# Kernel optimization log

Measured on AMD Instinct MI355X. Metric: run time of the kernel, lower is better.

## Reference

```python
import jax, jax.numpy as jnp
import numpy as np

POOL_LEN = 256
EPS = 1e-5
WEIGHT_BITS = 2


def adaptive_avg_pool1d(x, out_len):
    """Faithful torch AdaptiveAvgPool1d: window i = [floor(i*L/out), ceil((i+1)*L/out)).
    Implemented via cumsum + static gathers (jit-friendly, vectorized)."""
    L = x.shape[-1]
    i = np.arange(out_len)
    starts = (i * L) // out_len
    ends = -((-(i + 1) * L) // out_len)  # integer ceil
    csum = jnp.cumsum(x, axis=-1)
    csum = jnp.concatenate([jnp.zeros(x.shape[:-1] + (1,), x.dtype), csum], axis=-1)
    counts = jnp.asarray(ends - starts, x.dtype)
    return (csum[..., ends] - csum[..., starts]) / counts


def quantize_weight(w, bits=WEIGHT_BITS):
    """2-bit symmetric uniform quantization, per-output-channel scale, STE."""
    qp = 2 ** (bits - 1) - 1          # +1
    qn = -(2 ** (bits - 1))           # -2
    scale = jnp.maximum(jnp.max(jnp.abs(w), axis=1, keepdims=True) / qp, 1e-8)
    w_q = jnp.clip(jnp.round(w / scale), qn, qp) * scale
    return w + jax.lax.stop_gradient(w_q - w)  # straight-through estimator


def setup_inputs() -> dict:
    key = jax.random.key(0)
    k1, k2, k3, kw = jax.random.split(key, 4)
    B = 64
    return {
        "stage1": jax.random.normal(k1, (B, 256, 5000), jnp.float32),
        "stage2": jax.random.normal(k2, (B, 128, 2500), jnp.float32),
        "stage3": jax.random.normal(k3, (B, 64, 625), jnp.float32),
        "alpha": jnp.ones((3,), jnp.float32) / 3.0,
        "weight": jax.random.normal(kw, (128, 448), jnp.float32) * 0.05,
        "bias": jnp.zeros((128,), jnp.float32),
        "gamma": jnp.ones((128,), jnp.float32),
        "beta": jnp.zeros((128,), jnp.float32),
    }


def reference(stage1, stage2, stage3, alpha, weight, bias, gamma, beta):
    w = jax.nn.softmax(alpha)
    s1 = adaptive_avg_pool1d(stage1, POOL_LEN) * w[0]
    s2 = adaptive_avg_pool1d(stage2, POOL_LEN) * w[1]
    s3 = adaptive_avg_pool1d(stage3, POOL_LEN) * w[2]
    fused = jnp.concatenate([s1, s2, s3], axis=1)  # (B, 448, 256)
    wq = quantize_weight(weight)
    y = jnp.einsum('oc,bcl->bol', wq, fused) + bias[None, :, None]  # (B, 128, 256)
    # BatchNorm1d (training mode: batch stats over N and L)
    mean = jnp.mean(y, axis=(0, 2))
    var = jnp.var(y, axis=(0, 2))
    yn = (y - mean[None, :, None]) * jax.lax.rsqrt(var + EPS)[None, :, None]
    yn = yn * gamma[None, :, None] + beta[None, :, None]
    act = jax.nn.elu(yn)
    return jnp.mean(act, axis=-1)  # (B, 128)
```

## Files before the change

### kernel.cpp

```cpp
#include <hip/hip_runtime.h>
#include <hip/hip_bf16.h>

#define EPSV 1e-5f

typedef __attribute__((ext_vector_type(8))) short short8v;
typedef __attribute__((ext_vector_type(4))) short short4v;
typedef __attribute__((ext_vector_type(4))) float float4v;

__device__ inline unsigned short f2bf(float x) {
  __hip_bfloat16 h = __float2bfloat16(x);
  return *reinterpret_cast<unsigned short*>(&h);
}
__device__ inline float bf2f(unsigned short b) {
  unsigned u = ((unsigned)b) << 16;
  float f;
  __builtin_memcpy(&f, &u, 4);
  return f;
}

template <int L, int MAXW, int OPL>
__device__ __forceinline__ void windows_from_seg(
    const float* __restrict__ seg, int lbase, float wst,
    unsigned short* __restrict__ outp, int lane) {
  int sbase = (lbase * L) >> 8;
  unsigned short res[OPL];
  #pragma unroll
  for (int oo = 0; oo < OPL; ++oo) {
    int l = lbase + lane * OPL + oo;
    int start = ((l * L) >> 8) - sbase;
    int end = (((l + 1) * L + 255) >> 8) - sbase;
    int width = end - start;
    float s = 0.f;
    #pragma unroll
    for (int i = 0; i < MAXW; ++i) {
      float v = seg[start + i];
      s += (i < width) ? v : 0.f;
    }
    res[oo] = f2bf(s / (float)width * wst);
  }
  if (OPL == 2) {
    unsigned pk = ((unsigned)res[1] << 16) | res[0];
    *(unsigned*)(outp + lane * 2) = pk;
  } else {
    unsigned pk0 = ((unsigned)res[1] << 16) | res[0];
    unsigned pk1 = ((unsigned)res[3] << 16) | res[2];
    unsigned long long pk = ((unsigned long long)pk1 << 32) | pk0;
    *(unsigned long long*)(outp + lane * 4) = pk;
  }
}

template <int L, int SPAN, int MAXW, int OPL>
__device__ __forceinline__ void pool_span2_vec(
    const float* __restrict__ pA, const float* __restrict__ pB,
    int lbA, int lbB, float wst,
    unsigned short* __restrict__ outA, unsigned short* __restrict__ outB,
    float* __restrict__ seg, int lane) {
  constexpr int S4 = SPAN / 4;
  constexpr int NLD = (S4 + 63) / 64;
  float4v rA[NLD], rB[NLD];
  const float4v* gA = (const float4v*)pA;
  const float4v* gB = (const float4v*)pB;
  #pragma unroll
  for (int j = 0; j < NLD; ++j) {
    int idx = lane + 64 * j;
    if (NLD * 64 == S4 || idx < S4) rA[j] = __builtin_nontemporal_load(gA + idx);
  }
  #pragma unroll
  for (int j = 0; j < NLD; ++j) {
    int idx = lane + 64 * j;
    if (NLD * 64 == S4 || idx < S4) rB[j] = __builtin_nontemporal_load(gB + idx);
  }
  if (lane < MAXW + 3) seg[SPAN + lane] = 0.f;
  #pragma unroll
  for (int j = 0; j < NLD; ++j) {
    int idx = lane + 64 * j;
    if (NLD * 64 == S4 || idx < S4) *(float4v*)&seg[idx * 4] = rA[j];
  }
  windows_from_seg<L, MAXW, OPL>(seg, lbA, wst, outA, lane);
  #pragma unroll
  for (int j = 0; j < NLD; ++j) {
    int idx = lane + 64 * j;
    if (NLD * 64 == S4 || idx < S4) *(float4v*)&seg[idx * 4] = rB[j];
  }
  windows_from_seg<L, MAXW, OPL>(seg, lbB, wst, outB, lane);
}

template <int L, int SPAN, int MAXW, int OPL>
__device__ __forceinline__ void pool_span_scalar(
    const float* __restrict__ spanp, int lbase, float wst,
    unsigned short* __restrict__ outp, float* __restrict__ seg, int lane) {
  constexpr int NLD = (SPAN + 63) / 64;
  if (lane < MAXW + 3) seg[SPAN + lane] = 0.f;
  #pragma unroll
  for (int j = 0; j < NLD; ++j) {
    int idx = lane + 64 * j;
    if (idx < SPAN) seg[idx] = __builtin_nontemporal_load(spanp + idx);
  }
  windows_from_seg<L, MAXW, OPL>(seg, lbase, wst, outp, lane);
}

__global__ __launch_bounds__(256) void pool_quant_kernel(
    const float* __restrict__ s1, const float* __restrict__ s2,
    const float* __restrict__ s3, const float* __restrict__ alpha,
    const float* __restrict__ w, unsigned short* __restrict__ fusedb,
    unsigned short* __restrict__ qbf, float* __restrict__ scales) {
  __shared__ float pool_lds[4][2524];
  int bid = blockIdx.x;
  int t = threadIdx.x;
  int wv = t >> 6, lane = t & 63;

  if (bid >= 6144) {
    int o = bid - 6144;
    const float* wr = w + o * 448;
    float m = 0.f;
    for (int c = t; c < 448; c += 256) m = fmaxf(m, fabsf(wr[c]));
    float* sm = pool_lds[0];
    for (int off = 32; off; off >>= 1) m = fmaxf(m, __shfl_down(m, off, 64));
    if ((t & 63) == 0) sm[t >> 6] = m;
    __syncthreads();
    m = fmaxf(fmaxf(sm[0], sm[1]), fmaxf(sm[2], sm[3]));
    float scale = fmaxf(m, 1e-8f);
    for (int c = t; c < 448; c += 256) {
      float q = rintf(wr[c] / scale);
      q = fminf(fmaxf(q, -2.f), 1.f);
      qbf[o * 448 + c] = f2bf(q);
    }
    if (t == 0) scales[o] = scale;
    return;
  }

  float a0 = alpha[0], a1 = alpha[1], a2 = alpha[2];
  float mx = fmaxf(a0, fmaxf(a1, a2));
  float e0 = expf(a0 - mx), e1 = expf(a1 - mx), e2 = expf(a2 - mx);
  float esum = e0 + e1 + e2;
  float* seg = pool_lds[wv];

  if (bid < 4096) {
    int rr = bid * 4 + wv;
    int b = rr >> 8, c = rr & 255;
    const float* rowp = s1 + ((size_t)b * 256 + c) * 5000;
    unsigned short* outp = fusedb + ((size_t)b * 448 + c) * 256;
    pool_span2_vec<5000, 2500, 21, 2>(rowp, rowp + 2500, 0, 128, e0 / esum,
                                      outp, outp + 128, seg, lane);
  } else if (bid < 5120) {
    int wt = (bid - 4096) * 4 + wv;
    int rA = wt * 2, rB = rA + 1;
    int bA = rA >> 7, cA = rA & 127;
    int bB = rB >> 7, cB = rB & 127;
    const float* pA = s2 + ((size_t)bA * 128 + cA) * 2500;
    const float* pB = s2 + ((size_t)bB * 128 + cB) * 2500;
    unsigned short* oA = fusedb + ((size_t)bA * 448 + 256 + cA) * 256;
    unsigned short* oB = fusedb + ((size_t)bB * 448 + 256 + cB) * 256;
    pool_span2_vec<2500, 2500, 11, 4>(pA, pB, 0, 0, e1 / esum, oA, oB, seg, lane);
  } else {
    int u = (bid - 5120) * 4 + wv;
    int b = u >> 6, c = u & 63;
    const float* spanp = s3 + ((size_t)b * 64 + c) * 625;
    unsigned short* outp = fusedb + ((size_t)b * 448 + 384 + c) * 256;
    pool_span_scalar<625, 625, 4, 4>(spanp, 0, e2 / esum, outp, seg, lane);
  }
}

__global__ __launch_bounds__(256) void mfma_gemm_kernel(
    const unsigned short* __restrict__ qbf, const float* __restrict__ scales,
    const unsigned short* __restrict__ fusedb, const float* __restrict__ bias,
    unsigned short* __restrict__ ybf, float* __restrict__ Psum,
    float* __restrict__ Pssq) {
  __shared__ __align__(16) unsigned short Asm[64][40];
  __shared__ __align__(16) unsigned Bsm32[16][66];
  int b = blockIdx.z;
  int o0 = blockIdx.y * 64;
  int l0 = blockIdx.x * 64;
  int tid = threadIdx.x;
  int wave = tid >> 6, lane = tid & 63;
  int wm = wave >> 1, wn = wave & 1;
  int lrow = lane & 15, lg = lane >> 4;
  const unsigned short* Fp = fusedb + (size_t)b * 448 * 256;
  float4v acc[2][2];
  #pragma unroll
  for (int i = 0; i < 2; ++i)
    #pragma unroll
    for (int j = 0; j < 2; ++j) acc[i][j] = (float4v){0.f, 0.f, 0.f, 0.f};
  for (int c0 = 0; c0 < 448; c0 += 32) {
    { int r = tid >> 2, k0 = (tid & 3) * 8;
      *(short8v*)&Asm[r][k0] = *(const short8v*)(qbf + (size_t)(o0 + r) * 448 + c0 + k0); }
    { int kp = tid >> 4, n0 = (tid & 15) * 4;
      const unsigned short* g0 = Fp + (size_t)(c0 + 2 * kp) * 256 + l0 + n0;
      short4v v0 = *(const short4v*)g0;
      short4v v1 = *(const short4v*)(g0 + 256);
      #pragma unroll
      for (int j = 0; j < 4; ++j)
        Bsm32[kp][n0 + j] =
            (((unsigned)(unsigned short)v1[j]) << 16) | (unsigned short)v0[j];
    }
    __syncthreads();
    short8v af[2];
    #pragma unroll
    for (int mf = 0; mf < 2; ++mf)
      af[mf] = *(const short8v*)&Asm[wm * 32 + mf * 16 + lrow][lg * 8];
    #pragma unroll
    for (int nf = 0; nf < 2; ++nf) {
      int n = wn * 32 + nf * 16 + lrow;
      int tmp[4];
      #pragma unroll
      for (int jj = 0; jj < 4; ++jj) tmp[jj] = (int)Bsm32[lg * 4 + jj][n];
      short8v bf;
      __builtin_memcpy(&bf, tmp, 16);
      #pragma unroll
      for (int mf = 0; mf < 2; ++mf)
        acc[mf][nf] = __builtin_amdgcn_mfma_f32_16x16x32_bf16(af[mf], bf, acc[mf][nf], 0, 0, 0);
    }
    __syncthreads();
  }
  float sv[2][4], qv[2][4];
  #pragma unroll
  for (int mf = 0; mf < 2; ++mf) {
    #pragma unroll
    for (int reg = 0; reg < 4; ++reg) {
      int r = o0 + wm * 32 + mf * 16 + lg * 4 + reg;
      float sc = scales[r], bv = bias[r];
      float s = 0.f, q = 0.f;
      #pragma unroll
      for (int nf = 0; nf < 2; ++nf) {
        int col = l0 + wn * 32 + nf * 16 + lrow;
        float val = acc[mf][nf][reg] * sc + bv;
        ybf[((size_t)b * 128 + r) * 256 + col] = f2bf(val);
        s += val; q += val * val;
      }
      sv[mf][reg] = s; qv[mf][reg] = q;
    }
  }
  #pragma unroll
  for (int mf = 0; mf < 2; ++mf)
    #pragma unroll
    for (int reg = 0; reg < 4; ++reg)
      #pragma unroll
      for (int m = 1; m < 16; m <<= 1) {
        sv[mf][reg] += __shfl_xor(sv[mf][reg], m, 64);
        qv[mf][reg] += __shfl_xor(qv[mf][reg], m, 64);
      }
  if (lrow == 0) {
    int slot = b * 8 + blockIdx.x * 2 + wn;
    #pragma unroll
    for (int mf = 0; mf < 2; ++mf)
      #pragma unroll
      for (int reg = 0; reg < 4; ++reg) {
        int r = o0 + wm * 32 + mf * 16 + lg * 4 + reg;
        Psum[r * 512 + slot] = sv[mf][reg];
        Pssq[r * 512 + slot] = qv[mf][reg];
      }
  }
}

__global__ __launch_bounds__(256) void final_kernel(
    const unsigned short* __restrict__ ybf, const float* __restrict__ Psum,
    const float* __restrict__ Pssq, const float* __restrict__ gamma,
    const float* __restrict__ beta, float* __restrict__ out) {
  int w = threadIdx.x >> 6;
  int lane = threadIdx.x & 63;
  int bo = blockIdx.x * 4 + w;
  int o = bo & 127;

  float s = 0.f, q = 0.f;
  const float* Pp = Psum + o * 512 + lane * 8;
  const float* Qp = Pssq + o * 512 + lane * 8;
  #pragma unroll
  for (int i = 0; i < 8; ++i) { s += Pp[i]; q += Qp[i]; }
  #pragma unroll
  for (int m = 1; m < 64; m <<= 1) {
    s += __shfl_xor(s, m, 64);
    q += __shfl_xor(q, m, 64);
  }
  float mean = s * (1.f / 16384.f);
  float var = q * (1.f / 16384.f) - mean * mean;
  float rs = rsqrtf(var + EPSV);
  float a = rs * gamma[o];
  float bb = beta[o] - mean * a;

  ushort4 v = *(const ushort4*)(ybf + (size_t)bo * 256 + lane * 4);
  float acc = 0.f;
  #pragma unroll
  for (int j = 0; j < 4; ++j) {
    float e = bf2f((&v.x)[j]);
    float yn = e * a + bb;
    acc += yn > 0.f ? yn : expm1f(yn);
  }
  for (int m = 32; m; m >>= 1) acc += __shfl_down(acc, m, 64);
  if (lane == 0) out[bo] = acc * (1.f / 256.f);
}

extern "C" void kernel_launch(void* const* d_in, const int* in_sizes, int n_in,
                              void* d_out, int out_size, void* d_ws, size_t ws_size,
                              hipStream_t stream) {
  const float* s1     = (const float*)d_in[0];
  const float* s2     = (const float*)d_in[1];
  const float* s3     = (const float*)d_in[2];
  const float* alpha  = (const float*)d_in[3];
  const float* weight = (const float*)d_in[4];
  const float* bias   = (const float*)d_in[5];
  const float* gamma  = (const float*)d_in[6];
  const float* beta   = (const float*)d_in[7];
  float* out = (float*)d_out;

  char* ws = (char*)d_ws;
  unsigned short* fusedb = (unsigned short*)ws;
  unsigned short* qbf    = (unsigned short*)(ws + 14680064);
  float* scales          = (float*)(ws + 14794752);
  unsigned short* ybf    = (unsigned short*)(ws + 14795264);
  float* Psum            = (float*)(ws + 18989568);
  float* Pssq            = (float*)(ws + 19251712);

  pool_quant_kernel<<<6272, 256, 0, stream>>>(s1, s2, s3, alpha, weight,
                                              fusedb, qbf, scales);
  dim3 g(4, 2, 64);
  mfma_gemm_kernel<<<g, 256, 0, stream>>>(qbf, scales, fusedb, bias, ybf,
                                          Psum, Pssq);
  final_kernel<<<2048, 256, 0, stream>>>(ybf, Psum, Pssq, gamma, beta, out);
}
```

Before: 95.06 us.

## Split pooling rows into quarter/half spans per wave to raise occupancy

The pooling kernel now gives each wave a 1250-element span instead of two full 2500-element spans. Stage1 rows are split across the four waves of a block and stage2 rows across wave pairs, with float2 loads where the span offset is not 16-byte aligned. The LDS per block is roughly halved, launch bounds request 8 blocks per CU, and the grid grows to 21632 blocks. The goal is more memory-level parallelism and occupancy for the bandwidth-bound pooling step, at the cost of losing the double-buffered two-load-in-flight pattern per wave and launching many more blocks.

```diff
diff --git a/kernel.cpp b/kernel.cpp
--- a/kernel.cpp
+++ b/kernel.cpp
@@ -6,6 +6,7 @@
 typedef __attribute__((ext_vector_type(8))) short short8v;
 typedef __attribute__((ext_vector_type(4))) short short4v;
 typedef __attribute__((ext_vector_type(4))) float float4v;
+typedef __attribute__((ext_vector_type(2))) float float2v;
 
 __device__ inline unsigned short f2bf(float x) {
   __hip_bfloat16 h = __float2bfloat16(x);
@@ -38,7 +39,9 @@
     }
     res[oo] = f2bf(s / (float)width * wst);
   }
-  if (OPL == 2) {
+  if (OPL == 1) {
+    outp[lane] = res[0];
+  } else if (OPL == 2) {
     unsigned pk = ((unsigned)res[1] << 16) | res[0];
     *(unsigned*)(outp + lane * 2) = pk;
   } else {
@@ -49,68 +52,58 @@
   }
 }
 
-template <int L, int SPAN, int MAXW, int OPL>
-__device__ __forceinline__ void pool_span2_vec(
-    const float* __restrict__ pA, const float* __restrict__ pB,
-    int lbA, int lbB, float wst,
-    unsigned short* __restrict__ outA, unsigned short* __restrict__ outB,
-    float* __restrict__ seg, int lane) {
-  constexpr int S4 = SPAN / 4;
-  constexpr int NLD = (S4 + 63) / 64;
-  float4v rA[NLD], rB[NLD];
-  const float4v* gA = (const float4v*)pA;
-  const float4v* gB = (const float4v*)pB;
-  #pragma unroll
-  for (int j = 0; j < NLD; ++j) {
-    int idx = lane + 64 * j;
-    if (NLD * 64 == S4 || idx < S4) rA[j] = __builtin_nontemporal_load(gA + idx);
-  }
-  #pragma unroll
-  for (int j = 0; j < NLD; ++j) {
-    int idx = lane + 64 * j;
-    if (NLD * 64 == S4 || idx < S4) rB[j] = __builtin_nontemporal_load(gB + idx);
-  }
-  if (lane < MAXW + 3) seg[SPAN + lane] = 0.f;
-  #pragma unroll
-  for (int j = 0; j < NLD; ++j) {
-    int idx = lane + 64 * j;
-    if (NLD * 64 == S4 || idx < S4) *(float4v*)&seg[idx * 4] = rA[j];
-  }
-  windows_from_seg<L, MAXW, OPL>(seg, lbA, wst, outA, lane);
-  #pragma unroll
-  for (int j = 0; j < NLD; ++j) {
-    int idx = lane + 64 * j;
-    if (NLD * 64 == S4 || idx < S4) *(float4v*)&seg[idx * 4] = rB[j];
-  }
-  windows_from_seg<L, MAXW, OPL>(seg, lbB, wst, outB, lane);
-}
-
-template <int L, int SPAN, int MAXW, int OPL>
-__device__ __forceinline__ void pool_span_scalar(
+template <int L, int SPAN, int MAXW, int OPL, int VECW>
+__device__ __forceinline__ void pool_span(
     const float* __restrict__ spanp, int lbase, float wst,
     unsigned short* __restrict__ outp, float* __restrict__ seg, int lane) {
-  constexpr int NLD = (SPAN + 63) / 64;
-  if (lane < MAXW + 3) seg[SPAN + lane] = 0.f;
-  #pragma unroll
-  for (int j = 0; j < NLD; ++j) {
-    int idx = lane + 64 * j;
-    if (idx < SPAN) seg[idx] = __builtin_nontemporal_load(spanp + idx);
+  if (lane < MAXW) seg[SPAN + lane] = 0.f;
+  if (VECW == 4) {
+    constexpr int SV = SPAN / 4;
+    constexpr int NLD = (SV + 63) / 64;
+    const float4v* gp = (const float4v*)spanp;
+    #pragma unroll
+    for (int j = 0; j < NLD; ++j) {
+      int idx = lane + 64 * j;
+      if (NLD * 64 == SV || idx < SV) {
+        float4v v = __builtin_nontemporal_load(gp + idx);
+        *(float4v*)&seg[idx * 4] = v;
+      }
+    }
+  } else if (VECW == 2) {
+    constexpr int SV = SPAN / 2;
+    constexpr int NLD = (SV + 63) / 64;
+    const float2v* gp = (const float2v*)spanp;
+    #pragma unroll
+    for (int j = 0; j < NLD; ++j) {
+      int idx = lane + 64 * j;
+      if (NLD * 64 == SV || idx < SV) {
+        float2v v = __builtin_nontemporal_load(gp + idx);
+        *(float2v*)&seg[idx * 2] = v;
+      }
+    }
+  } else {
+    constexpr int NLD = (SPAN + 63) / 64;
+    #pragma unroll
+    for (int j = 0; j < NLD; ++j) {
+      int idx = lane + 64 * j;
+      if (idx < SPAN) seg[idx] = __builtin_nontemporal_load(spanp + idx);
+    }
   }
   windows_from_seg<L, MAXW, OPL>(seg, lbase, wst, outp, lane);
 }
 
-__global__ __launch_bounds__(256) void pool_quant_kernel(
+__global__ __launch_bounds__(256, 8) void pool_quant_kernel(
     const float* __restrict__ s1, const float* __restrict__ s2,
     const float* __restrict__ s3, const float* __restrict__ alpha,
     const float* __restrict__ w, unsigned short* __restrict__ fusedb,
     unsigned short* __restrict__ qbf, float* __restrict__ scales) {
-  __shared__ float pool_lds[4][2524];
+  __shared__ float pool_lds[4][1280];
   int bid = blockIdx.x;
   int t = threadIdx.x;
   int wv = t >> 6, lane = t & 63;
 
-  if (bid >= 6144) {
-    int o = bid - 6144;
+  if (bid >= 21504) {
+    int o = bid - 21504;
     const float* wr = w + o * 448;
     float m = 0.f;
     for (int c = t; c < 448; c += 256) m = fmaxf(m, fabsf(wr[c]));
@@ -135,29 +128,34 @@
   float esum = e0 + e1 + e2;
   float* seg = pool_lds[wv];
 
-  if (bid < 4096) {
-    int rr = bid * 4 + wv;
-    int b = rr >> 8, c = rr & 255;
+  if (bid < 16384) {
+    int b = bid >> 8, c = bid & 255;
     const float* rowp = s1 + ((size_t)b * 256 + c) * 5000;
-    unsigned short* outp = fusedb + ((size_t)b * 448 + c) * 256;
-    pool_span2_vec<5000, 2500, 21, 2>(rowp, rowp + 2500, 0, 128, e0 / esum,
-                                      outp, outp + 128, seg, lane);
-  } else if (bid < 5120) {
-    int wt = (bid - 4096) * 4 + wv;
-    int rA = wt * 2, rB = rA + 1;
-    int bA = rA >> 7, cA = rA & 127;
-    int bB = rB >> 7, cB = rB & 127;
-    const float* pA = s2 + ((size_t)bA * 128 + cA) * 2500;
-    const float* pB = s2 + ((size_t)bB * 128 + cB) * 2500;
-    unsigned short* oA = fusedb + ((size_t)bA * 448 + 256 + cA) * 256;
-    unsigned short* oB = fusedb + ((size_t)bB * 448 + 256 + cB) * 256;
-    pool_span2_vec<2500, 2500, 11, 4>(pA, pB, 0, 0, e1 / esum, oA, oB, seg, lane);
+    unsigned short* outr = fusedb + ((size_t)b * 448 + c) * 256;
+    const float* spanp = rowp + wv * 1250;
+    unsigned short* outp = outr + wv * 64;
+    int lbase = wv * 64;
+    if (wv & 1)
+      pool_span<5000, 1250, 21, 1, 2>(spanp, lbase, e0 / esum, outp, seg, lane);
+    else
+      pool_span<5000, 1250, 21, 1, 4>(spanp, lbase, e0 / esum, outp, seg, lane);
+  } else if (bid < 20480) {
+    int r = (bid - 16384) * 2 + (wv >> 1);
+    int h = wv & 1;
+    int b = r >> 7, c = r & 127;
+    const float* spanp = s2 + ((size_t)b * 128 + c) * 2500 + h * 1250;
+    unsigned short* outp = fusedb + ((size_t)b * 448 + 256 + c) * 256 + h * 128;
+    int lbase = h * 128;
+    if (h)
+      pool_span<2500, 1250, 11, 2, 2>(spanp, lbase, e1 / esum, outp, seg, lane);
+    else
+      pool_span<2500, 1250, 11, 2, 4>(spanp, lbase, e1 / esum, outp, seg, lane);
   } else {
-    int u = (bid - 5120) * 4 + wv;
+    int u = (bid - 20480) * 4 + wv;
     int b = u >> 6, c = u & 63;
     const float* spanp = s3 + ((size_t)b * 64 + c) * 625;
     unsigned short* outp = fusedb + ((size_t)b * 448 + 384 + c) * 256;
-    pool_span_scalar<625, 625, 4, 4>(spanp, 0, e2 / esum, outp, seg, lane);
+    pool_span<625, 625, 4, 4, 1>(spanp, 0, e2 / esum, outp, seg, lane);
   }
 }
 
@@ -310,8 +308,8 @@
   float* Psum            = (float*)(ws + 18989568);
   float* Pssq            = (float*)(ws + 19251712);
 
-  pool_quant_kernel<<<6272, 256, 0, stream>>>(s1, s2, s3, alpha, weight,
-                                              fusedb, qbf, scales);
+  pool_quant_kernel<<<21632, 256, 0, stream>>>(s1, s2, s3, alpha, weight,
+                                               fusedb, qbf, scales);
   dim3 g(4, 2, 64);
   mfma_gemm_kernel<<<g, 256, 0, stream>>>(qbf, scales, fusedb, bias, ybf,
                                           Psum, Pssq);
```

Measured after the change: 95.00 us. About the same (-0.1%).
